# Performance work log

Hardware: AMD Instinct MI355X
Metric: run time of the kernel (lower is better)

Reference implementation:

```python
import jax, jax.numpy as jnp
import numpy as np

B, S, H = 4, 16, 4096          # batch, new query tokens, hidden
NH, NKV, HD = 32, 8, 128       # query heads, kv heads, head_dim
PAST = 8192                    # cached kv length
ROPE_BASE = 10000.0


def setup_inputs() -> dict:
    key = jax.random.key(0)
    ks = jax.random.split(key, 7)
    wscale = 0.02
    hidden_states = jax.random.normal(ks[0], (B, S, H), jnp.float32)
    k_cache = jax.random.normal(ks[1], (B, PAST, NKV, HD), jnp.float32)
    v_cache = jax.random.normal(ks[2], (B, PAST, NKV, HD), jnp.float32)
    Wq = jax.random.normal(ks[3], (H, NH * HD), jnp.float32) * wscale
    Wk = jax.random.normal(ks[4], (H, NKV * HD), jnp.float32) * wscale
    Wv = jax.random.normal(ks[5], (H, NKV * HD), jnp.float32) * wscale
    Wo = jax.random.normal(ks[6], (NH * HD, H), jnp.float32) * wscale
    position_ids = PAST + jnp.tile(jnp.arange(S, dtype=jnp.int32)[None, :], (B, 1))
    return {"hidden_states": hidden_states, "k_cache": k_cache, "v_cache": v_cache,
            "Wq": Wq, "Wk": Wk, "Wv": Wv, "Wo": Wo, "position_ids": position_ids}


def _rotate_half(x):
    h = x.shape[-1] // 2
    return jnp.concatenate([-x[..., h:], x[..., :h]], axis=-1)


def reference(hidden_states, k_cache, v_cache, Wq, Wk, Wv, Wo, position_ids):
    b, s, _ = hidden_states.shape
    # projections -> [b, heads, s, hd]
    q = (hidden_states @ Wq).reshape(b, s, NH, HD).transpose(0, 2, 1, 3)
    k = (hidden_states @ Wk).reshape(b, s, NKV, HD).transpose(0, 2, 1, 3)
    v = (hidden_states @ Wv).reshape(b, s, NKV, HD).transpose(0, 2, 1, 3)
    # RoPE (LlamaRotaryEmbedding: base=10000, half-split rotate)
    inv_freq = 1.0 / (ROPE_BASE ** (jnp.arange(0, HD, 2, dtype=jnp.float32) / HD))
    ang = position_ids.astype(jnp.float32)[..., None] * inv_freq      # [b, s, hd/2]
    emb = jnp.concatenate([ang, ang], axis=-1)                        # [b, s, hd]
    cos = jnp.cos(emb)[:, None]                                       # [b, 1, s, hd]
    sin = jnp.sin(emb)[:, None]
    q = q * cos + _rotate_half(q) * sin
    k = k * cos + _rotate_half(k) * sin
    # kv-cache concat: cache stored [b, past, nkv, hd] -> [b, nkv, K, hd]
    k_all = jnp.concatenate([k_cache.transpose(0, 2, 1, 3), k], axis=2)
    v_all = jnp.concatenate([v_cache.transpose(0, 2, 1, 3), v], axis=2)
    # GQA repeat_kv (repeat_interleave along head dim)
    n_rep = NH // NKV
    k_all = jnp.repeat(k_all, n_rep, axis=1)                          # [b, NH, K, hd]
    v_all = jnp.repeat(v_all, n_rep, axis=1)
    K = k_all.shape[2]
    scale = HD ** -0.5
    scores = jnp.einsum('bhqd,bhkd->bhqk', q, k_all) * scale          # [b, NH, s, K]
    # flash varlen causal with seqlen_q < seqlen_k: bottom-right aligned mask
    allow = jnp.arange(K)[None, :] <= (K - s + jnp.arange(s))[:, None]
    scores = jnp.where(allow, scores, jnp.float32(-1e30))
    probs = jax.nn.softmax(scores, axis=-1)
    attn = jnp.einsum('bhqk,bhkd->bhqd', probs, v_all)                # [b, NH, s, hd]
    attn = attn.transpose(0, 2, 1, 3).reshape(b, s, NH * HD)
    return attn @ Wo
```

## Files before the change

### kernel.cpp

```cpp
#include <hip/hip_runtime.h>

#define BB 4
#define SS 16
#define NH 32
#define NKV 8
#define HD 128
#define PAST 8192
#define KVLEN 8208
#define KSPLIT 8
#define ASPLIT 16
#define CHUNK 513
#define NTILE 9

typedef __attribute__((ext_vector_type(8))) short short8;
typedef __attribute__((ext_vector_type(4))) float f32x4;

__device__ __forceinline__ unsigned short f2bf(float f) {
  unsigned u = __float_as_uint(f);
  u = (u + 0x7FFFu + ((u >> 16) & 1u)) >> 16;
  return (unsigned short)u;
}
__device__ __forceinline__ float bf2f(unsigned short h) {
  return __uint_as_float(((unsigned)h) << 16);
}
__device__ __forceinline__ unsigned cvtpk(float lo, float hi) {
  unsigned r;
  asm("v_cvt_pk_bf16_f32 %0, %1, %2" : "=v"(r) : "v"(lo), "v"(hi));
  return r;
}
__device__ __forceinline__ void st8(void* p, unsigned lo, unsigned hi) {
  *(unsigned long long*)p = (unsigned long long)lo | ((unsigned long long)hi << 32);
}
__device__ __forceinline__ float getc(const float4& v, int c) {
  return c == 0 ? v.x : c == 1 ? v.y : c == 2 ? v.z : v.w;
}
__device__ __forceinline__ int imin(int a, int b) { return a < b ? a : b; }
__device__ __forceinline__ int imax(int a, int b) { return a > b ? a : b; }

__device__ __forceinline__ void bar_lds() {
  asm volatile("s_waitcnt lgkmcnt(0)" ::: "memory");
  __builtin_amdgcn_s_barrier();
  asm volatile("" ::: "memory");
}
__device__ __forceinline__ void wait_lds() {
  asm volatile("s_waitcnt lgkmcnt(0)" ::: "memory");
}

__global__ __launch_bounds__(256) void xconv(const float* __restrict__ X,
                                             unsigned short* __restrict__ XB) {
  int gid = blockIdx.x * 256 + threadIdx.x;
  float4 v = *(const float4*)&X[(size_t)gid * 4];
  ushort4 pk;
  pk.x = f2bf(v.x); pk.y = f2bf(v.y); pk.z = f2bf(v.z); pk.w = f2bf(v.w);
  *(ushort4*)&XB[(size_t)gid * 4] = pk;
}

__global__ __launch_bounds__(256) void gemm_skinny(
    const unsigned short* __restrict__ A,
    const float* __restrict__ W0, const float* __restrict__ W1, const float* __restrict__ W2,
    int nw0, int nw1, int nw2,
    float* __restrict__ part, int Ntot, int kchunk) {
  __shared__ unsigned short Wt[64 * 64];
  const int nt = blockIdx.x, ks = blockIdx.y;
  const int tid = threadIdx.x, lane = tid & 63, w = tid >> 6;
  const int lr = lane & 15, lc = lane >> 4;
  const int n0 = nt * 64;
  const float* W; int wld, wcol;
  if (n0 < nw0) { W = W0; wld = nw0; wcol = n0; }
  else if (n0 < nw0 + nw1) { W = W1; wld = nw1; wcol = n0 - nw0; }
  else { W = W2; wld = nw2; wcol = n0 - nw0 - nw1; }

  f32x4 acc[4];
  #pragma unroll
  for (int mi = 0; mi < 4; ++mi)
    #pragma unroll
    for (int i = 0; i < 4; ++i) acc[mi][i] = 0.f;

  const int qn = tid & 15, qk = tid >> 4;
  const int kb0 = ks * kchunk;
  const int nkt = kchunk / 64;

  float4 wr0, wr1, wr2, wr3;
  {
    const float* wp = &W[(size_t)(kb0 + qk * 4) * wld + wcol + qn * 4];
    wr0 = *(const float4*)(wp);
    wr1 = *(const float4*)(wp + wld);
    wr2 = *(const float4*)(wp + 2 * (size_t)wld);
    wr3 = *(const float4*)(wp + 3 * (size_t)wld);
  }

  for (int kt = 0; kt < nkt; ++kt) {
    const int kb = kb0 + kt * 64;
    #pragma unroll
    for (int c = 0; c < 4; ++c) {
      const int n = qn * 4 + c;
      ushort4 pk;
      pk.x = f2bf(getc(wr0, c)); pk.y = f2bf(getc(wr1, c));
      pk.z = f2bf(getc(wr2, c)); pk.w = f2bf(getc(wr3, c));
      const int byt = n * 128 + ((qk * 8) ^ ((n & 7) << 4));
      *(ushort4*)((char*)Wt + byt) = pk;
    }
    bar_lds();
    if (kt + 1 < nkt) {
      const float* wp = &W[(size_t)(kb + 64 + qk * 4) * wld + wcol + qn * 4];
      wr0 = *(const float4*)(wp);
      wr1 = *(const float4*)(wp + wld);
      wr2 = *(const float4*)(wp + 2 * (size_t)wld);
      wr3 = *(const float4*)(wp + 3 * (size_t)wld);
    }
    #pragma unroll
    for (int kh = 0; kh < 2; ++kh) {
      const int ncol = w * 16 + lr;
      short8 bf = *(const short8*)((char*)Wt + ncol * 128 + ((kh * 64 + lc * 16) ^ ((ncol & 7) << 4)));
      const int kkg = kb + kh * 32 + lc * 8;
      #pragma unroll
      for (int mi = 0; mi < 4; ++mi) {
        short8 af = *(const short8*)&A[(size_t)(mi * 16 + lr) * 4096 + kkg];
        acc[mi] = __builtin_amdgcn_mfma_f32_16x16x32_bf16(af, bf, acc[mi], 0, 0, 0);
      }
    }
    bar_lds();
  }
  #pragma unroll
  for (int mi = 0; mi < 4; ++mi)
    #pragma unroll
    for (int i = 0; i < 4; ++i) {
      const int row = mi * 16 + lc * 4 + i;
      part[((size_t)ks * 64 + row) * Ntot + n0 + w * 16 + lr] = acc[mi][i];
    }
}

__global__ __launch_bounds__(256) void proj_reduce(
    const float* __restrict__ part, const int* __restrict__ posids,
    unsigned short* __restrict__ QR, float* __restrict__ KF,
    float* __restrict__ VF) {
  const int gid = blockIdx.x * 256 + threadIdx.x;
  const int j = gid & 63;
  const int hh = (gid >> 6) % 48;
  const int row = gid / 3072;
  const int b = row >> 4, s = row & 15;
  int col0; bool rope;
  if (hh < 32)      { col0 = hh * 128 + j; rope = true; }
  else if (hh < 40) { col0 = 4096 + (hh - 32) * 128 + j; rope = true; }
  else              { col0 = 5120 + (hh - 40) * 128 + j; rope = false; }
  float v0 = 0.f, v1 = 0.f;
  #pragma unroll
  for (int ks = 0; ks < KSPLIT; ++ks) {
    v0 += part[((size_t)ks * 64 + row) * 6144 + col0];
    v1 += part[((size_t)ks * 64 + row) * 6144 + col0 + 64];
  }
  float o0 = v0, o1 = v1;
  if (rope) {
    const int pos = posids[row];
    const double inv = exp2(-(double)j * (13.287712379549449 / 64.0));
    double th = (double)pos * inv;
    const double TWO_PI = 6.283185307179586476925286766559;
    th -= floor(th / TWO_PI) * TWO_PI;
    float sv, cv;
    sincosf((float)th, &sv, &cv);
    o0 = v0 * cv - v1 * sv;
    o1 = v1 * cv + v0 * sv;
  }
  if (hh < 32) {
    const size_t didx = (((size_t)(b * 32 + hh) * 16 + s) * 128) + j;
    QR[didx] = f2bf(o0);
    QR[didx + 64] = f2bf(o1);
  } else if (hh < 40) {
    const size_t didx = (((size_t)(b * 8 + (hh - 32)) * 16 + s) * 128) + j;
    KF[didx] = o0;
    KF[didx + 64] = o1;
  } else {
    const size_t didx = (((size_t)(b * 8 + (hh - 40)) * 16 + s) * 128) + j;
    VF[didx] = o0;
    VF[didx + 64] = o1;
  }
}

__global__ __launch_bounds__(256, 2) void attn_kernel(
    const float* __restrict__ kc, const float* __restrict__ vc,
    const unsigned short* __restrict__ QR, const float* __restrict__ KF,
    const float* __restrict__ VF,
    float* __restrict__ Opart, float* __restrict__ ML) {
  __shared__ unsigned short Klds[2][64 * 136];
  __shared__ unsigned short Vt[2][128 * 64];
  __shared__ unsigned short Plds[4][16 * 72];

  const int split = blockIdx.x, kvh = blockIdx.y, b = blockIdx.z;
  const int tid = threadIdx.x, lane = tid & 63, w = tid >> 6;
  const int lr = lane & 15, lc = lane >> 4;

  const int kstart = split * CHUNK;
  const int dl = (tid & 31) * 4;
  const int rk = tid >> 5;

  const float* kc_base = kc + (((size_t)b * PAST) * NKV + kvh) * HD + dl;
  const float* vc_base = vc + (((size_t)b * PAST) * NKV + kvh) * HD + dl;
  const float* kf_base = KF + (((size_t)b * NKV + kvh) * SS) * HD + dl;
  const float* vf_base = VF + (((size_t)b * NKV + kvh) * SS) * HD + dl;

  float4 kpre[8];
  float4 vpre[2][4];

  auto load_K = [&](int kk0) {
    #pragma unroll
    for (int pass = 0; pass < 8; ++pass) {
      const int kk = kk0 + pass * 8 + rk;
      const int ts = imin(imax(kk - PAST, 0), SS - 1);
      const float* p = (kk < PAST) ? (kc_base + (size_t)kk * (NKV * HD))
                                   : (kf_base + (size_t)ts * HD);
      kpre[pass] = *(const float4*)p;
    }
  };
  auto load_V = [&](int kk0) {
    #pragma unroll
    for (int pp = 0; pp < 2; ++pp)
      #pragma unroll
      for (int jj = 0; jj < 4; ++jj) {
        const int kk = kk0 + rk * 8 + pp * 4 + jj;
        const int ts = imin(imax(kk - PAST, 0), SS - 1);
        const float* p = (kk < PAST) ? (vc_base + (size_t)kk * (NKV * HD))
                                     : (vf_base + (size_t)ts * HD);
        vpre[pp][jj] = *(const float4*)p;
      }
  };

  auto store_tile = [&](int buf) {
    #pragma unroll
    for (int pass = 0; pass < 8; ++pass) {
      const int kr = pass * 8 + rk;
      const float4 f = kpre[pass];
      st8((char*)&Klds[buf][0] + kr * 272 + dl * 2,
          cvtpk(f.x, f.y), cvtpk(f.z, f.w));
    }
    #pragma unroll
    for (int pp = 0; pp < 2; ++pp) {
      const int krb = rk * 8 + pp * 4;
      #pragma unroll
      for (int c = 0; c < 4; ++c) {
        const int d = dl + c;
        const int g = ((d ^ (d >> 3)) & 7) << 4;
        st8((char*)&Vt[buf][0] + d * 128 + ((krb * 2) ^ g),
            cvtpk(getc(vpre[pp][0], c), getc(vpre[pp][1], c)),
            cvtpk(getc(vpre[pp][2], c), getc(vpre[pp][3], c)));
      }
    }
  };

  short8 qf[4];
  {
    const unsigned short* qb = QR + (((size_t)b * NH + kvh * 4 + w) * SS + lr) * HD;
    #pragma unroll
    for (int kd = 0; kd < 4; ++kd) qf[kd] = *(const short8*)(qb + kd * 32 + lc * 8);
  }
  asm volatile("" :: "v"(qf[0]), "v"(qf[1]), "v"(qf[2]), "v"(qf[3]));

  load_K(kstart);
  load_V(kstart);
  store_tile(0);
  bar_lds();

  float m_i[4], l_i[4];
  f32x4 oacc[8];
  #pragma unroll
  for (int i = 0; i < 4; ++i) { m_i[i] = -1e30f; l_i[i] = 0.f; }
  #pragma unroll
  for (int d8 = 0; d8 < 8; ++d8)
    #pragma unroll
    for (int i = 0; i < 4; ++i) oacc[d8][i] = 0.f;

  for (int t = 0; t < NTILE; ++t) {
    const int buf = t & 1;
    const int kk0 = kstart + t * 64;
    const int nvalid = imin(64, kstart + CHUNK - kk0);

    if (t + 1 < NTILE) {
      load_K(kk0 + 64);
      __builtin_amdgcn_sched_barrier(0);
    }

    f32x4 sacc[4];
    #pragma unroll
    for (int nb = 0; nb < 4; ++nb)
      #pragma unroll
      for (int i = 0; i < 4; ++i) sacc[nb][i] = 0.f;
    #pragma unroll
    for (int kd = 0; kd < 4; ++kd) {
      #pragma unroll
      for (int nb = 0; nb < 4; ++nb) {
        const int key = nb * 16 + lr;
        short8 bf = *(const short8*)((char*)&Klds[buf][0] + key * 272 + kd * 64 + lc * 16);
        sacc[nb] = __builtin_amdgcn_mfma_f32_16x16x32_bf16(qf[kd], bf, sacc[nb], 0, 0, 0);
      }
    }

    if (t + 1 < NTILE) {
      load_V(kk0 + 64);
      __builtin_amdgcn_sched_barrier(0);
    }

    const float scl = 0.08838834764831845f;
    float resc[4];
    #pragma unroll
    for (int i = 0; i < 4; ++i) {
      const int s = lc * 4 + i;
      float vv[4];
      #pragma unroll
      for (int nb = 0; nb < 4; ++nb) {
        const int klocal = nb * 16 + lr;
        const int kk = kk0 + klocal;
        const bool ok = (klocal < nvalid) && (kk <= PAST + s);
        vv[nb] = ok ? sacc[nb][i] * scl : -1e30f;
      }
      float mx = fmaxf(fmaxf(vv[0], vv[1]), fmaxf(vv[2], vv[3]));
      mx = fmaxf(mx, __shfl_xor(mx, 1));
      mx = fmaxf(mx, __shfl_xor(mx, 2));
      mx = fmaxf(mx, __shfl_xor(mx, 4));
      mx = fmaxf(mx, __shfl_xor(mx, 8));
      const float mnew = fmaxf(m_i[i], mx);
      const float rs = __expf(m_i[i] - mnew);
      float p0 = __expf(vv[0] - mnew), p1 = __expf(vv[1] - mnew);
      float p2 = __expf(vv[2] - mnew), p3 = __expf(vv[3] - mnew);
      float sum = p0 + p1 + p2 + p3;
      sum += __shfl_xor(sum, 1);
      sum += __shfl_xor(sum, 2);
      sum += __shfl_xor(sum, 4);
      sum += __shfl_xor(sum, 8);
      l_i[i] = l_i[i] * rs + sum;
      m_i[i] = mnew;
      resc[i] = rs;
      unsigned short* prow = &Plds[w][s * 72];
      prow[0 * 16 + lr] = f2bf(p0);
      prow[1 * 16 + lr] = f2bf(p1);
      prow[2 * 16 + lr] = f2bf(p2);
      prow[3 * 16 + lr] = f2bf(p3);
    }
    #pragma unroll
    for (int d8 = 0; d8 < 8; ++d8)
      #pragma unroll
      for (int i = 0; i < 4; ++i) oacc[d8][i] *= resc[i];

    wait_lds();

    #pragma unroll
    for (int ks2 = 0; ks2 < 2; ++ks2) {
      short8 pf = *(const short8*)((char*)&Plds[w][0] + lr * 144 + ks2 * 64 + lc * 16);
      #pragma unroll
      for (int db = 0; db < 8; ++db) {
        const int d = db * 16 + lr;
        const int g = ((d ^ (d >> 3)) & 7) << 4;
        short8 vf = *(const short8*)((char*)&Vt[buf][0] + d * 128 + ((ks2 * 64 + lc * 16) ^ g));
        oacc[db] = __builtin_amdgcn_mfma_f32_16x16x32_bf16(pf, vf, oacc[db], 0, 0, 0);
      }
    }

    if (t + 1 < NTILE) store_tile(buf ^ 1);
    bar_lds();
  }

  const size_t pbase = (((size_t)b * NKV + kvh) * ASPLIT + split) * 64;
  #pragma unroll
  for (int db = 0; db < 8; ++db)
    #pragma unroll
    for (int i = 0; i < 4; ++i) {
      const int row = w * 16 + lc * 4 + i;
      Opart[(pbase + row) * HD + db * 16 + lr] = oacc[db][i];
    }
  if (lr == 0) {
    #pragma unroll
    for (int i = 0; i < 4; ++i) {
      const int row = w * 16 + lc * 4 + i;
      ML[(pbase + row) * 2] = m_i[i];
      ML[(pbase + row) * 2 + 1] = l_i[i];
    }
  }
}

__global__ __launch_bounds__(128) void combine(const float* __restrict__ Opart,
                                               const float* __restrict__ ML,
                                               unsigned short* __restrict__ AT) {
  const int rid = blockIdx.x;
  const int d = threadIdx.x;
  const int s = rid & 15, h = (rid >> 4) & 31, b = rid >> 9;
  const int kvh = h >> 2, g = h & 3;
  const int prow = g * 16 + s;
  const size_t base = ((size_t)b * NKV + kvh) * ASPLIT;
  float ms[ASPLIT], ls[ASPLIT];
  float M = -1e30f;
  #pragma unroll
  for (int sp = 0; sp < ASPLIT; ++sp) {
    ms[sp] = ML[((base + sp) * 64 + prow) * 2];
    ls[sp] = ML[((base + sp) * 64 + prow) * 2 + 1];
    M = fmaxf(M, ms[sp]);
  }
  float denom = 0.f, acc = 0.f;
  #pragma unroll
  for (int sp = 0; sp < ASPLIT; ++sp) {
    const float e = __expf(ms[sp] - M);
    denom += ls[sp] * e;
    acc += e * Opart[((base + sp) * 64 + prow) * HD + d];
  }
  AT[((size_t)(b * 16 + s)) * 4096 + h * 128 + d] = f2bf(acc / denom);
}

__global__ __launch_bounds__(256) void wo_reduce(const float* __restrict__ part,
                                                 float* __restrict__ out) {
  const int gid = blockIdx.x * 256 + threadIdx.x;
  float4 s = {0, 0, 0, 0};
  #pragma unroll
  for (int ks = 0; ks < KSPLIT; ++ks) {
    const float4 v = *(const float4*)&part[(size_t)ks * 262144 + (size_t)gid * 4];
    s.x += v.x; s.y += v.y; s.z += v.z; s.w += v.w;
  }
  *(float4*)&out[(size_t)gid * 4] = s;
}

extern "C" void kernel_launch(void* const* d_in, const int* in_sizes, int n_in,
                              void* d_out, int out_size, void* d_ws, size_t ws_size,
                              hipStream_t stream) {
  (void)in_sizes; (void)n_in; (void)out_size; (void)ws_size;
  const float* hs = (const float*)d_in[0];
  const float* kc = (const float*)d_in[1];
  const float* vc = (const float*)d_in[2];
  const float* Wq = (const float*)d_in[3];
  const float* Wk = (const float*)d_in[4];
  const float* Wv = (const float*)d_in[5];
  const float* Wo = (const float*)d_in[6];
  const int* pos = (const int*)d_in[7];
  float* out = (float*)d_out;
  char* ws = (char*)d_ws;

  unsigned short* XB = (unsigned short*)(ws);
  unsigned short* QR = (unsigned short*)(ws + 0x080000);
  float* KF = (float*)(ws + 0x100000);
  float* VF = (float*)(ws + 0x140000);
  unsigned short* AT = (unsigned short*)(ws + 0x180000);
  float* RED = (float*)(ws + 0x200000);
  float* ML  = (float*)(ws + 0x1300000);

  hipLaunchKernelGGL(xconv, dim3(256), dim3(256), 0, stream, hs, XB);
  hipLaunchKernelGGL(gemm_skinny, dim3(96, KSPLIT), dim3(256), 0, stream,
                     XB, Wq, Wk, Wv, 4096, 1024, 1024, RED, 6144, 4096 / KSPLIT);
  hipLaunchKernelGGL(proj_reduce, dim3(768), dim3(256), 0, stream, RED, pos, QR, KF, VF);
  hipLaunchKernelGGL(attn_kernel, dim3(ASPLIT, NKV, BB), dim3(256), 0, stream,
                     kc, vc, QR, KF, VF, RED, ML);
  hipLaunchKernelGGL(combine, dim3(2048), dim3(128), 0, stream, RED, ML, AT);
  hipLaunchKernelGGL(gemm_skinny, dim3(64, KSPLIT), dim3(256), 0, stream,
                     AT, Wo, Wo, Wo, 4096, 0, 0, RED, 4096, 4096 / KSPLIT);
  hipLaunchKernelGGL(wo_reduce, dim3(256), dim3(256), 0, stream, RED, out);
}
```

Before: 138.5 us.

## Warp-specialize attention into producer waves loading KV and consumer MFMA waves

Doubles the attention block to 512 threads: the upper 256 threads act as producers that load fp32 K/V tiles from global memory, convert them to bf16 and write the next LDS buffer, while the lower 256 threads run the QK MFMA, online softmax and PV MFMA. Both groups meet at the same block barrier each tile. The aim is to take global-load latency and conversion work off the compute waves' critical path. In exchange each block uses more waves, which may limit how many blocks fit per CU, and there is still a full barrier every tile.

```diff
diff --git a/kernel.cpp b/kernel.cpp
--- a/kernel.cpp
+++ b/kernel.cpp
@@ -176,7 +176,7 @@
   }
 }
 
-__global__ __launch_bounds__(256, 2) void attn_kernel(
+__global__ __launch_bounds__(512, 2) void attn_kernel(
     const float* __restrict__ kc, const float* __restrict__ vc,
     const unsigned short* __restrict__ QR, const float* __restrict__ KF,
     const float* __restrict__ VF,
@@ -186,191 +186,178 @@
   __shared__ unsigned short Plds[4][16 * 72];
 
   const int split = blockIdx.x, kvh = blockIdx.y, b = blockIdx.z;
-  const int tid = threadIdx.x, lane = tid & 63, w = tid >> 6;
-  const int lr = lane & 15, lc = lane >> 4;
-
+  const int tid = threadIdx.x;
   const int kstart = split * CHUNK;
-  const int dl = (tid & 31) * 4;
-  const int rk = tid >> 5;
-
-  const float* kc_base = kc + (((size_t)b * PAST) * NKV + kvh) * HD + dl;
-  const float* vc_base = vc + (((size_t)b * PAST) * NKV + kvh) * HD + dl;
-  const float* kf_base = KF + (((size_t)b * NKV + kvh) * SS) * HD + dl;
-  const float* vf_base = VF + (((size_t)b * NKV + kvh) * SS) * HD + dl;
-
-  float4 kpre[8];
-  float4 vpre[2][4];
-
-  auto load_K = [&](int kk0) {
-    #pragma unroll
-    for (int pass = 0; pass < 8; ++pass) {
-      const int kk = kk0 + pass * 8 + rk;
-      const int ts = imin(imax(kk - PAST, 0), SS - 1);
-      const float* p = (kk < PAST) ? (kc_base + (size_t)kk * (NKV * HD))
-                                   : (kf_base + (size_t)ts * HD);
-      kpre[pass] = *(const float4*)p;
-    }
-  };
-  auto load_V = [&](int kk0) {
-    #pragma unroll
-    for (int pp = 0; pp < 2; ++pp)
-      #pragma unroll
-      for (int jj = 0; jj < 4; ++jj) {
-        const int kk = kk0 + rk * 8 + pp * 4 + jj;
+
+  if (tid >= 256) {
+    const int ptid = tid - 256;
+    const int dl = (ptid & 31) * 4;
+    const int rk = ptid >> 5;
+    const float* kc_base = kc + (((size_t)b * PAST) * NKV + kvh) * HD + dl;
+    const float* vc_base = vc + (((size_t)b * PAST) * NKV + kvh) * HD + dl;
+    const float* kf_base = KF + (((size_t)b * NKV + kvh) * SS) * HD + dl;
+    const float* vf_base = VF + (((size_t)b * NKV + kvh) * SS) * HD + dl;
+
+    auto stage = [&](int kk0, int buf) {
+      float4 kpre[8];
+      float4 vpre[8];
+      #pragma unroll
+      for (int pass = 0; pass < 8; ++pass) {
+        const int kk = kk0 + pass * 8 + rk;
+        const int ts = imin(imax(kk - PAST, 0), SS - 1);
+        const float* p = (kk < PAST) ? (kc_base + (size_t)kk * (NKV * HD))
+                                     : (kf_base + (size_t)ts * HD);
+        kpre[pass] = *(const float4*)p;
+      }
+      #pragma unroll
+      for (int j = 0; j < 8; ++j) {
+        const int kk = kk0 + rk * 8 + j;
         const int ts = imin(imax(kk - PAST, 0), SS - 1);
         const float* p = (kk < PAST) ? (vc_base + (size_t)kk * (NKV * HD))
                                      : (vf_base + (size_t)ts * HD);
-        vpre[pp][jj] = *(const float4*)p;
-      }
-  };
-
-  auto store_tile = [&](int buf) {
-    #pragma unroll
-    for (int pass = 0; pass < 8; ++pass) {
-      const int kr = pass * 8 + rk;
-      const float4 f = kpre[pass];
-      st8((char*)&Klds[buf][0] + kr * 272 + dl * 2,
-          cvtpk(f.x, f.y), cvtpk(f.z, f.w));
-    }
-    #pragma unroll
-    for (int pp = 0; pp < 2; ++pp) {
-      const int krb = rk * 8 + pp * 4;
-      #pragma unroll
-      for (int c = 0; c < 4; ++c) {
-        const int d = dl + c;
-        const int g = ((d ^ (d >> 3)) & 7) << 4;
-        st8((char*)&Vt[buf][0] + d * 128 + ((krb * 2) ^ g),
-            cvtpk(getc(vpre[pp][0], c), getc(vpre[pp][1], c)),
-            cvtpk(getc(vpre[pp][2], c), getc(vpre[pp][3], c)));
-      }
-    }
-  };
-
-  short8 qf[4];
-  {
-    const unsigned short* qb = QR + (((size_t)b * NH + kvh * 4 + w) * SS + lr) * HD;
-    #pragma unroll
-    for (int kd = 0; kd < 4; ++kd) qf[kd] = *(const short8*)(qb + kd * 32 + lc * 8);
-  }
-  asm volatile("" :: "v"(qf[0]), "v"(qf[1]), "v"(qf[2]), "v"(qf[3]));
-
-  load_K(kstart);
-  load_V(kstart);
-  store_tile(0);
-  bar_lds();
-
-  float m_i[4], l_i[4];
-  f32x4 oacc[8];
-  #pragma unroll
-  for (int i = 0; i < 4; ++i) { m_i[i] = -1e30f; l_i[i] = 0.f; }
-  #pragma unroll
-  for (int d8 = 0; d8 < 8; ++d8)
-    #pragma unroll
-    for (int i = 0; i < 4; ++i) oacc[d8][i] = 0.f;
-
-  for (int t = 0; t < NTILE; ++t) {
-    const int buf = t & 1;
-    const int kk0 = kstart + t * 64;
-    const int nvalid = imin(64, kstart + CHUNK - kk0);
-
-    if (t + 1 < NTILE) {
-      load_K(kk0 + 64);
-      __builtin_amdgcn_sched_barrier(0);
-    }
-
-    f32x4 sacc[4];
-    #pragma unroll
-    for (int nb = 0; nb < 4; ++nb)
-      #pragma unroll
-      for (int i = 0; i < 4; ++i) sacc[nb][i] = 0.f;
-    #pragma unroll
-    for (int kd = 0; kd < 4; ++kd) {
-      #pragma unroll
-      for (int nb = 0; nb < 4; ++nb) {
-        const int key = nb * 16 + lr;
-        short8 bf = *(const short8*)((char*)&Klds[buf][0] + key * 272 + kd * 64 + lc * 16);
-        sacc[nb] = __builtin_amdgcn_mfma_f32_16x16x32_bf16(qf[kd], bf, sacc[nb], 0, 0, 0);
-      }
-    }
-
-    if (t + 1 < NTILE) {
-      load_V(kk0 + 64);
-      __builtin_amdgcn_sched_barrier(0);
-    }
-
-    const float scl = 0.08838834764831845f;
-    float resc[4];
-    #pragma unroll
-    for (int i = 0; i < 4; ++i) {
-      const int s = lc * 4 + i;
-      float vv[4];
-      #pragma unroll
-      for (int nb = 0; nb < 4; ++nb) {
-        const int klocal = nb * 16 + lr;
-        const int kk = kk0 + klocal;
-        const bool ok = (klocal < nvalid) && (kk <= PAST + s);
-        vv[nb] = ok ? sacc[nb][i] * scl : -1e30f;
-      }
-      float mx = fmaxf(fmaxf(vv[0], vv[1]), fmaxf(vv[2], vv[3]));
-      mx = fmaxf(mx, __shfl_xor(mx, 1));
-      mx = fmaxf(mx, __shfl_xor(mx, 2));
-      mx = fmaxf(mx, __shfl_xor(mx, 4));
-      mx = fmaxf(mx, __shfl_xor(mx, 8));
-      const float mnew = fmaxf(m_i[i], mx);
-      const float rs = __expf(m_i[i] - mnew);
-      float p0 = __expf(vv[0] - mnew), p1 = __expf(vv[1] - mnew);
-      float p2 = __expf(vv[2] - mnew), p3 = __expf(vv[3] - mnew);
-      float sum = p0 + p1 + p2 + p3;
-      sum += __shfl_xor(sum, 1);
-      sum += __shfl_xor(sum, 2);
-      sum += __shfl_xor(sum, 4);
-      sum += __shfl_xor(sum, 8);
-      l_i[i] = l_i[i] * rs + sum;
-      m_i[i] = mnew;
-      resc[i] = rs;
-      unsigned short* prow = &Plds[w][s * 72];
-      prow[0 * 16 + lr] = f2bf(p0);
-      prow[1 * 16 + lr] = f2bf(p1);
-      prow[2 * 16 + lr] = f2bf(p2);
-      prow[3 * 16 + lr] = f2bf(p3);
-    }
+        vpre[j] = *(const float4*)p;
+      }
+      #pragma unroll
+      for (int pass = 0; pass < 8; ++pass) {
+        const int kr = pass * 8 + rk;
+        st8((char*)&Klds[buf][0] + kr * 272 + dl * 2,
+            cvtpk(kpre[pass].x, kpre[pass].y), cvtpk(kpre[pass].z, kpre[pass].w));
+      }
+      #pragma unroll
+      for (int pp = 0; pp < 2; ++pp) {
+        const int krb = rk * 8 + pp * 4;
+        #pragma unroll
+        for (int c = 0; c < 4; ++c) {
+          const int d = dl + c;
+          const int g = ((d ^ (d >> 3)) & 7) << 4;
+          st8((char*)&Vt[buf][0] + d * 128 + ((krb * 2) ^ g),
+              cvtpk(getc(vpre[pp * 4 + 0], c), getc(vpre[pp * 4 + 1], c)),
+              cvtpk(getc(vpre[pp * 4 + 2], c), getc(vpre[pp * 4 + 3], c)));
+        }
+      }
+    };
+
+    stage(kstart, 0);
+    bar_lds();
+    for (int t = 0; t < NTILE; ++t) {
+      if (t + 1 < NTILE) stage(kstart + (t + 1) * 64, (t + 1) & 1);
+      bar_lds();
+    }
+  } else {
+    const int lane = tid & 63, w = tid >> 6;
+    const int lr = lane & 15, lc = lane >> 4;
+
+    short8 qf[4];
+    {
+      const unsigned short* qb = QR + (((size_t)b * NH + kvh * 4 + w) * SS + lr) * HD;
+      #pragma unroll
+      for (int kd = 0; kd < 4; ++kd) qf[kd] = *(const short8*)(qb + kd * 32 + lc * 8);
+    }
+
+    float m_i[4], l_i[4];
+    f32x4 oacc[8];
+    #pragma unroll
+    for (int i = 0; i < 4; ++i) { m_i[i] = -1e30f; l_i[i] = 0.f; }
     #pragma unroll
     for (int d8 = 0; d8 < 8; ++d8)
       #pragma unroll
-      for (int i = 0; i < 4; ++i) oacc[d8][i] *= resc[i];
-
-    wait_lds();
-
-    #pragma unroll
-    for (int ks2 = 0; ks2 < 2; ++ks2) {
-      short8 pf = *(const short8*)((char*)&Plds[w][0] + lr * 144 + ks2 * 64 + lc * 16);
-      #pragma unroll
-      for (int db = 0; db < 8; ++db) {
-        const int d = db * 16 + lr;
-        const int g = ((d ^ (d >> 3)) & 7) << 4;
-        short8 vf = *(const short8*)((char*)&Vt[buf][0] + d * 128 + ((ks2 * 64 + lc * 16) ^ g));
-        oacc[db] = __builtin_amdgcn_mfma_f32_16x16x32_bf16(pf, vf, oacc[db], 0, 0, 0);
-      }
-    }
-
-    if (t + 1 < NTILE) store_tile(buf ^ 1);
+      for (int i = 0; i < 4; ++i) oacc[d8][i] = 0.f;
+
     bar_lds();
-  }
-
-  const size_t pbase = (((size_t)b * NKV + kvh) * ASPLIT + split) * 64;
-  #pragma unroll
-  for (int db = 0; db < 8; ++db)
-    #pragma unroll
-    for (int i = 0; i < 4; ++i) {
-      const int row = w * 16 + lc * 4 + i;
-      Opart[(pbase + row) * HD + db * 16 + lr] = oacc[db][i];
-    }
-  if (lr == 0) {
-    #pragma unroll
-    for (int i = 0; i < 4; ++i) {
-      const int row = w * 16 + lc * 4 + i;
-      ML[(pbase + row) * 2] = m_i[i];
-      ML[(pbase + row) * 2 + 1] = l_i[i];
+
+    for (int t = 0; t < NTILE; ++t) {
+      const int buf = t & 1;
+      const int kk0 = kstart + t * 64;
+      const int nvalid = imin(64, kstart + CHUNK - kk0);
+
+      f32x4 sacc[4];
+      #pragma unroll
+      for (int nb = 0; nb < 4; ++nb)
+        #pragma unroll
+        for (int i = 0; i < 4; ++i) sacc[nb][i] = 0.f;
+      #pragma unroll
+      for (int kd = 0; kd < 4; ++kd) {
+        #pragma unroll
+        for (int nb = 0; nb < 4; ++nb) {
+          const int key = nb * 16 + lr;
+          short8 bf = *(const short8*)((char*)&Klds[buf][0] + key * 272 + kd * 64 + lc * 16);
+          sacc[nb] = __builtin_amdgcn_mfma_f32_16x16x32_bf16(qf[kd], bf, sacc[nb], 0, 0, 0);
+        }
+      }
+
+      const float scl = 0.08838834764831845f;
+      float resc[4];
+      #pragma unroll
+      for (int i = 0; i < 4; ++i) {
+        const int s = lc * 4 + i;
+        float vv[4];
+        #pragma unroll
+        for (int nb = 0; nb < 4; ++nb) {
+          const int klocal = nb * 16 + lr;
+          const int kk = kk0 + klocal;
+          const bool ok = (klocal < nvalid) && (kk <= PAST + s);
+          vv[nb] = ok ? sacc[nb][i] * scl : -1e30f;
+        }
+        float mx = fmaxf(fmaxf(vv[0], vv[1]), fmaxf(vv[2], vv[3]));
+        mx = fmaxf(mx, __shfl_xor(mx, 1));
+        mx = fmaxf(mx, __shfl_xor(mx, 2));
+        mx = fmaxf(mx, __shfl_xor(mx, 4));
+        mx = fmaxf(mx, __shfl_xor(mx, 8));
+        const float mnew = fmaxf(m_i[i], mx);
+        const float rs = __expf(m_i[i] - mnew);
+        float p0 = __expf(vv[0] - mnew), p1 = __expf(vv[1] - mnew);
+        float p2 = __expf(vv[2] - mnew), p3 = __expf(vv[3] - mnew);
+        float sum = p0 + p1 + p2 + p3;
+        sum += __shfl_xor(sum, 1);
+        sum += __shfl_xor(sum, 2);
+        sum += __shfl_xor(sum, 4);
+        sum += __shfl_xor(sum, 8);
+        l_i[i] = l_i[i] * rs + sum;
+        m_i[i] = mnew;
+        resc[i] = rs;
+        unsigned short* prow = &Plds[w][s * 72];
+        prow[0 * 16 + lr] = f2bf(p0);
+        prow[1 * 16 + lr] = f2bf(p1);
+        prow[2 * 16 + lr] = f2bf(p2);
+        prow[3 * 16 + lr] = f2bf(p3);
+      }
+      #pragma unroll
+      for (int d8 = 0; d8 < 8; ++d8)
+        #pragma unroll
+        for (int i = 0; i < 4; ++i) oacc[d8][i] *= resc[i];
+
+      wait_lds();
+
+      #pragma unroll
+      for (int ks2 = 0; ks2 < 2; ++ks2) {
+        short8 pf = *(const short8*)((char*)&Plds[w][0] + lr * 144 + ks2 * 64 + lc * 16);
+        #pragma unroll
+        for (int db = 0; db < 8; ++db) {
+          const int d = db * 16 + lr;
+          const int g = ((d ^ (d >> 3)) & 7) << 4;
+          short8 vf = *(const short8*)((char*)&Vt[buf][0] + d * 128 + ((ks2 * 64 + lc * 16) ^ g));
+          oacc[db] = __builtin_amdgcn_mfma_f32_16x16x32_bf16(pf, vf, oacc[db], 0, 0, 0);
+        }
+      }
+
+      bar_lds();
+    }
+
+    const size_t pbase = (((size_t)b * NKV + kvh) * ASPLIT + split) * 64;
+    #pragma unroll
+    for (int db = 0; db < 8; ++db)
+      #pragma unroll
+      for (int i = 0; i < 4; ++i) {
+        const int row = w * 16 + lc * 4 + i;
+        Opart[(pbase + row) * HD + db * 16 + lr] = oacc[db][i];
+      }
+    if (lr == 0) {
+      #pragma unroll
+      for (int i = 0; i < 4; ++i) {
+        const int row = w * 16 + lc * 4 + i;
+        ML[(pbase + row) * 2] = m_i[i];
+        ML[(pbase + row) * 2 + 1] = l_i[i];
+      }
     }
   }
 }
@@ -441,7 +428,7 @@
   hipLaunchKernelGGL(gemm_skinny, dim3(96, KSPLIT), dim3(256), 0, stream,
                      XB, Wq, Wk, Wv, 4096, 1024, 1024, RED, 6144, 4096 / KSPLIT);
   hipLaunchKernelGGL(proj_reduce, dim3(768), dim3(256), 0, stream, RED, pos, QR, KF, VF);
-  hipLaunchKernelGGL(attn_kernel, dim3(ASPLIT, NKV, BB), dim3(256), 0, stream,
+  hipLaunchKernelGGL(attn_kernel, dim3(ASPLIT, NKV, BB), dim3(512), 0, stream,
                      kc, vc, QR, KF, VF, RED, ML);
   hipLaunchKernelGGL(combine, dim3(2048), dim3(128), 0, stream, RED, ML, AT);
   hipLaunchKernelGGL(gemm_skinny, dim3(64, KSPLIT), dim3(256), 0, stream,
```

Measured after the change: 137.1 us. About the same (-1.0%).
